# Optimization experiments

Hardware: AMD Instinct MI355X
Metric: run time of the kernel (lower is better)

## Reference

```python
import jax, jax.numpy as jnp
import numpy as np

N = 16384        # total atoms
E = 262144       # edges
D = 128          # dim_embedding
F = 128          # num_filters
G = 50           # num_gaussians
L = 4            # num_interactions
CUTOFF = 5.0
GAMMA = 4.0
NUM_MOLS = 32
LOG2 = float(np.log(2.0))


def ssp(x):
    # ShiftedSoftplus: softplus(x) - log(2)
    return jax.nn.softplus(x) - LOG2


def setup_inputs() -> dict:
    key = jax.random.key(0)
    ks = jax.random.split(key, 24)
    s = lambda *sh: 1.0 / np.sqrt(sh[-2]) if len(sh) >= 2 else 0.1
    inp = {
        "z": jax.random.normal(ks[0], (N, 1), jnp.float32),
        "pos": jax.random.uniform(ks[1], (N, 3), jnp.float32),
        "batch": jnp.sort(jax.random.randint(ks[2], (N,), 0, NUM_MOLS)),
        "edge_src": jax.random.randint(ks[3], (E,), 0, N),
        "edge_dst": jax.random.randint(ks[4], (E,), 0, N),
        # embedding Linear(1, D)
        "emb_W": jax.random.normal(ks[5], (1, D), jnp.float32),
        "emb_b": jax.random.normal(ks[6], (D,), jnp.float32) * 0.1,
        # per-interaction stacked params [L, ...]
        "mlp_W1": jax.random.normal(ks[7], (L, G, F), jnp.float32) / np.sqrt(G),
        "mlp_b1": jnp.zeros((L, F), jnp.float32),
        "mlp_W2": jax.random.normal(ks[8], (L, F, F), jnp.float32) / np.sqrt(F),
        "mlp_b2": jnp.zeros((L, F), jnp.float32),
        "cf1_W": jax.random.normal(ks[9], (L, D, F), jnp.float32) / np.sqrt(D),   # CFConv.lin1 (no bias)
        "cf2_W": jax.random.normal(ks[10], (L, F, D), jnp.float32) / np.sqrt(F),  # CFConv.lin2
        "cf2_b": jnp.zeros((L, D), jnp.float32),
        "int_lin_W": jax.random.normal(ks[11], (L, D, D), jnp.float32) / np.sqrt(D),
        "int_lin_b": jnp.zeros((L, D), jnp.float32),
        # readout head
        "lin1_W": jax.random.normal(ks[12], (D, D // 2), jnp.float32) / np.sqrt(D),
        "lin1_b": jnp.zeros((D // 2,), jnp.float32),
        "lin2_W": jax.random.normal(ks[13], (D // 2, 1), jnp.float32) / np.sqrt(D // 2),
        "lin2_b": jnp.zeros((1,), jnp.float32),
    }
    return inp


def reference(z, pos, batch, edge_src, edge_dst, emb_W, emb_b,
              mlp_W1, mlp_b1, mlp_W2, mlp_b2, cf1_W, cf2_W, cf2_b,
              int_lin_W, int_lin_b, lin1_W, lin1_b, lin2_W, lin2_b):
    # atom embedding: Linear(1, D)
    h = z @ emb_W + emb_b                                  # [N, D]

    # interaction graph distances (graph connectivity precomputed)
    diff = pos[edge_src] - pos[edge_dst]                   # [E, 3]
    dist = jnp.sqrt(jnp.sum(diff * diff, axis=-1) + 1e-12) # [E]

    # radial basis expansion
    mu = jnp.linspace(0.0, CUTOFF, G).astype(h.dtype)      # [G]
    rbf = jnp.exp(-GAMMA * (dist[:, None] - mu) ** 2)      # [E, G]

    # cosine cutoff envelope
    C = 0.5 * (jnp.cos(dist * (np.pi / CUTOFF)) + 1.0)     # [E]

    for l in range(L):
        # continuous filter from RBF: MLP [E,G] -> [E,F]
        Wf = ssp(rbf @ mlp_W1[l] + mlp_b1[l]) @ mlp_W2[l] + mlp_b2[l]
        Wf = Wf * C[:, None]                               # [E, F]
        # CFConv: gather - multiply - scatter-add
        xj = (h @ cf1_W[l])[edge_src]                      # [E, F]
        agg = jax.ops.segment_sum(xj * Wf, edge_dst, num_segments=N)  # [N, F]
        x = agg @ cf2_W[l] + cf2_b[l]                      # [N, D]
        x = ssp(x)
        x = x @ int_lin_W[l] + int_lin_b[l]
        h = h + x                                          # residual

    h = ssp(h @ lin1_W + lin1_b) @ lin2_W + lin2_b         # [N, 1]
    out = jax.ops.segment_sum(h, batch, num_segments=NUM_MOLS)  # [NUM_MOLS, 1]
    return out
```

## Files before the change

kernel.cpp:

```cpp
#include <hip/hip_runtime.h>
#include <hip/hip_bf16.h>
#include <math.h>

#define N_ATOMS 16384
#define N_EDGES 262144
#define DIM 128
#define NF 128
#define NG 50
#define NL 4
#define NMOLS 32
#define EW 8

typedef short bf16x8 __attribute__((ext_vector_type(8)));
typedef float f32x4 __attribute__((ext_vector_type(4)));

__device__ __forceinline__ float ssp_f(float x) {
    float e = __expf(-fabsf(x));
    return fmaxf(x, 0.0f) + __logf(1.0f + e) - 0.6931471805599453f;
}

__device__ __forceinline__ short f2bf(float x) {
    __hip_bfloat16 b = __float2bfloat16(x);
    return *reinterpret_cast<short*>(&b);
}

__device__ __forceinline__ float bf2f(unsigned short u) {
    unsigned int v = ((unsigned int)u) << 16;
    return __builtin_bit_cast(float, v);
}

__global__ __launch_bounds__(512)
void k_embed_geom(const float* __restrict__ z, const float* __restrict__ Wv,
                  const float* __restrict__ bv, float* __restrict__ h,
                  const float* __restrict__ pos, const int* __restrict__ src,
                  const int* __restrict__ dst, float* __restrict__ dist,
                  float* __restrict__ Cenv, int* __restrict__ deg) {
    int idx = blockIdx.x * 512 + threadIdx.x;
    int n = idx >> 7, d = idx & 127;
    h[idx] = z[n] * Wv[d] + bv[d];
    if (blockIdx.x < N_EDGES / 512) {
        int e = blockIdx.x * 512 + threadIdx.x;
        int s = src[e], t = dst[e];
        float dx = pos[3*s]   - pos[3*t];
        float dy = pos[3*s+1] - pos[3*t+1];
        float dz = pos[3*s+2] - pos[3*t+2];
        float dd = sqrtf(dx*dx + dy*dy + dz*dz + 1e-12f);
        dist[e] = dd;
        Cenv[e] = 0.5f * (cosf(dd * (float)(M_PI / 5.0)) + 1.0f);
        atomicAdd(&deg[t], 1);
    }
}

__global__ __launch_bounds__(1024)
void k_scan(const int* __restrict__ deg, int* __restrict__ cur) {
    __shared__ int tot[1024];
    int t = threadIdx.x;
    int v[16];
    int s = 0;
    #pragma unroll
    for (int j = 0; j < 16; ++j) { int x = deg[t * 16 + j]; v[j] = s; s += x; }
    tot[t] = s;
    __syncthreads();
    for (int off = 1; off < 1024; off <<= 1) {
        int add = (t >= off) ? tot[t - off] : 0;
        __syncthreads();
        tot[t] += add;
        __syncthreads();
    }
    int base = (t == 0) ? 0 : tot[t - 1];
    #pragma unroll
    for (int j = 0; j < 16; ++j) cur[t * 16 + j] = base + v[j];
}

__global__ void k_fill(const int* __restrict__ dst, int* __restrict__ cur,
                       int* __restrict__ edge_of) {
    int e = blockIdx.x * blockDim.x + threadIdx.x;
    if (e < N_EDGES) {
        int p = atomicAdd(&cur[dst[e]], 1);
        edge_of[p] = e;
    }
}

__global__ __launch_bounds__(512)
void k_perm_rbf(const int* __restrict__ edge_of, const float* __restrict__ dist,
                const float* __restrict__ Cenv, const int* __restrict__ src,
                const int* __restrict__ dst, float* __restrict__ CenvS,
                int* __restrict__ srcS, int* __restrict__ dstS,
                short* __restrict__ rbfF) {
    int p = blockIdx.x * blockDim.x + threadIdx.x;
    if (p >= N_EDGES) return;
    int e = edge_of[p];
    float d = dist[e];
    CenvS[p] = Cenv[e];
    srcS[p]  = src[e];
    dstS[p]  = dst[e];
    int t = p >> 4, m = p & 15;
    #pragma unroll
    for (int kc = 0; kc < 2; ++kc) {
        #pragma unroll
        for (int q = 0; q < 4; ++q) {
            bf16x8 v;
            #pragma unroll
            for (int j = 0; j < 8; ++j) {
                float mu = (float)(kc * 32 + q * 8 + j) * (5.0f / 49.0f);
                float tt = d - mu;
                v[j] = f2bf(__expf(-4.0f * tt * tt));
            }
            *(bf16x8*)&rbfF[(size_t)((t * 2 + kc) * 64 + q * 16 + m) * 8] = v;
        }
    }
}

__global__ __launch_bounds__(512, 4)
void k_edge_csr(const short* __restrict__ rbfF, const float* __restrict__ CenvS,
                const int* __restrict__ srcS, const int* __restrict__ dstS,
                const float* __restrict__ W1, const float* __restrict__ b1,
                const float* __restrict__ W2, const float* __restrict__ b2,
                const unsigned short* __restrict__ xjb, float* __restrict__ agg)
{
    __shared__ short H1s[64 * 128];
    __shared__ unsigned short msgt[64][136];
    __shared__ int dsts[64];
    __shared__ unsigned long long maskS;
    const int tid  = threadIdx.x;
    const int lane = tid & 63;
    const int w    = tid >> 6;
    const int q    = lane >> 4;
    const int m    = lane & 15;

    bf16x8 W1R[2], W2R[4];
    #pragma unroll
    for (int kc = 0; kc < 2; ++kc) {
        bf16x8 f;
        #pragma unroll
        for (int j = 0; j < 8; ++j) {
            int k = kc * 32 + q * 8 + j;
            float v = (k < NG) ? W1[k * NF + w * 16 + m] : 0.0f;
            f[j] = f2bf(v);
        }
        W1R[kc] = f;
    }
    #pragma unroll
    for (int kc = 0; kc < 4; ++kc) {
        bf16x8 f;
        #pragma unroll
        for (int j = 0; j < 8; ++j) {
            int k = kc * 32 + q * 8 + j;
            f[j] = f2bf(W2[k * NF + w * 16 + m]);
        }
        W2R[kc] = f;
    }
    const float b1v = b1[w * 16 + m];
    const float b2v = b2[w * 16 + m];

    const int nrounds = N_EDGES / 64;
    for (int r = blockIdx.x; r < nrounds; r += gridDim.x) {
        const int p0 = r * 64;
        short* H = H1s;

        #pragma unroll
        for (int a = 0; a < 4; ++a) {
            int tile = r * 4 + a;
            f32x4 acc = {b1v, b1v, b1v, b1v};
            #pragma unroll
            for (int kc = 0; kc < 2; ++kc) {
                bf16x8 A = *(const bf16x8*)&rbfF[(size_t)((tile * 2 + kc) * 64 + lane) * 8];
                acc = __builtin_amdgcn_mfma_f32_16x16x32_bf16(A, W1R[kc], acc, 0, 0, 0);
            }
            #pragma unroll
            for (int i = 0; i < 4; ++i) {
                int e = a * 16 + q * 4 + i;
                int f = w * 16 + m;
                int byte = (e * 256 + f * 2) ^ ((e & 7) << 4);
                *(short*)((char*)H + byte) = f2bf(ssp_f(acc[i]));
            }
        }
        __syncthreads();

        unsigned short xu[4][4];
        #pragma unroll
        for (int a = 0; a < 4; ++a) {
            int4 s4 = *(const int4*)&srcS[p0 + a * 16 + q * 4];
            #pragma unroll
            for (int i = 0; i < 4; ++i)
                xu[a][i] = xjb[(size_t)((const int*)&s4)[i] * NF + w * 16 + m];
        }

        f32x4 acc2[4];
        #pragma unroll
        for (int a = 0; a < 4; ++a) {
            f32x4 acc = {b2v, b2v, b2v, b2v};
            #pragma unroll
            for (int kc = 0; kc < 4; ++kc) {
                int e = a * 16 + m;
                int byte = (e * 256 + (kc * 32 + q * 8) * 2) ^ ((e & 7) << 4);
                bf16x8 A = *(const bf16x8*)((const char*)H + byte);
                acc = __builtin_amdgcn_mfma_f32_16x16x32_bf16(A, W2R[kc], acc, 0, 0, 0);
            }
            acc2[a] = acc;
        }

        #pragma unroll
        for (int a = 0; a < 4; ++a) {
            float4 cc4 = *(const float4*)&CenvS[p0 + a * 16 + q * 4];
            #pragma unroll
            for (int i = 0; i < 4; ++i) {
                float v = acc2[a][i] * ((const float*)&cc4)[i];
                msgt[a * 16 + q * 4 + i][w * 16 + m] =
                    (unsigned short)f2bf(v * bf2f(xu[a][i]));
            }
        }
        if (w == 0) {
            int d = dstS[p0 + lane];
            int prev = __shfl_up(d, 1);
            bool head = (lane == 0) || (d != prev);
            unsigned long long mk = __ballot(head);
            dsts[lane] = d;
            if (lane == 0) maskS = mk;
        }
        __syncthreads();

        {
            int f = tid & 127;
            int g = tid >> 7;
            unsigned long long mm = maskS;
            int k = 0;
            while (mm) {
                int start = __ffsll(mm) - 1;
                mm &= mm - 1;
                int end = mm ? (__ffsll(mm) - 1) : 64;
                if ((k & 3) == g) {
                    float s0 = 0.0f, s1 = 0.0f, s2 = 0.0f, s3 = 0.0f;
                    int p = start;
                    for (; p + 4 <= end; p += 4) {
                        s0 += bf2f(msgt[p    ][f]);
                        s1 += bf2f(msgt[p + 1][f]);
                        s2 += bf2f(msgt[p + 2][f]);
                        s3 += bf2f(msgt[p + 3][f]);
                    }
                    for (; p < end; ++p) s0 += bf2f(msgt[p][f]);
                    float s = (s0 + s1) + (s2 + s3);
                    float* addr = &agg[(size_t)dsts[start] * NF + f];
                    if (start == 0 || end == 64) atomicAdd(addr, s);
                    else *addr = s;
                }
                ++k;
            }
        }
    }
}

template<int ACT, int RESID, int OUTBF>
__global__ __launch_bounds__(512, 2)
void k_node_mfma(const float* __restrict__ in, const float* __restrict__ W,
                 const float* __restrict__ bias, const float* __restrict__ resid,
                 void* __restrict__ outv, float* __restrict__ aggz)
{
    __shared__ short T[32 * 128];
    const int tid  = threadIdx.x;
    const int lane = tid & 63;
    const int w    = tid >> 6;
    const int q    = lane >> 4;
    const int m    = lane & 15;

    bf16x8 WR[4];
    #pragma unroll
    for (int kc = 0; kc < 4; ++kc) {
        bf16x8 f;
        #pragma unroll
        for (int j = 0; j < 8; ++j)
            f[j] = f2bf(W[(kc * 32 + q * 8 + j) * DIM + w * 16 + m]);
        WR[kc] = f;
    }
    const float bv = bias ? bias[w * 16 + m] : 0.0f;

    const int r0 = blockIdx.x * 32;

    {
        int row = tid >> 4;
        int k0  = (tid & 15) * 8;
        const float* src = in + (size_t)(r0 + row) * DIM + k0;
        float4 v0 = *(const float4*)(src);
        float4 v1 = *(const float4*)(src + 4);
        bf16x8 lo;
        #pragma unroll
        for (int j = 0; j < 4; ++j) {
            lo[j]     = f2bf(((const float*)&v0)[j]);
            lo[j + 4] = f2bf(((const float*)&v1)[j]);
        }
        int b0 = (row * 256 + k0 * 2) ^ ((row & 7) << 4);
        *(bf16x8*)((char*)T + b0) = lo;
        if (aggz) {
            float4 zz = {0.0f, 0.0f, 0.0f, 0.0f};
            float* dz = aggz + (size_t)(r0 + row) * DIM + k0;
            *(float4*)dz = zz;
            *(float4*)(dz + 4) = zz;
        }
    }
    __syncthreads();

    #pragma unroll
    for (int a = 0; a < 2; ++a) {
        f32x4 acc = {bv, bv, bv, bv};
        int row = a * 16 + m;
        #pragma unroll
        for (int kc = 0; kc < 4; ++kc) {
            int byte = (row * 256 + (kc * 32 + q * 8) * 2) ^ ((row & 7) << 4);
            bf16x8 A = *(const bf16x8*)((const char*)T + byte);
            acc = __builtin_amdgcn_mfma_f32_16x16x32_bf16(A, WR[kc], acc, 0, 0, 0);
        }
        #pragma unroll
        for (int i = 0; i < 4; ++i) {
            float v = acc[i];
            if (ACT) v = ssp_f(v);
            size_t oi = (size_t)(r0 + a * 16 + q * 4 + i) * DIM + w * 16 + m;
            if (RESID) v += resid[oi];
            if (OUTBF) ((unsigned short*)outv)[oi] = (unsigned short)f2bf(v);
            else       ((float*)outv)[oi] = v;
        }
    }
}

template<int EMIT, int FINAL>
__global__ __launch_bounds__(512, 2)
void k_node_fused(const float* __restrict__ agg, const float* __restrict__ W2,
                  const float* __restrict__ b2, const float* __restrict__ Wi,
                  const float* __restrict__ bi, float* __restrict__ h,
                  const float* __restrict__ W1n, unsigned short* __restrict__ xjn,
                  float* __restrict__ aggz,
                  const float* __restrict__ l1W, const float* __restrict__ l1B,
                  const float* __restrict__ l2W, const float* __restrict__ l2b,
                  const int* __restrict__ batch, float* __restrict__ out)
{
    __shared__ short T[32 * 128];
    __shared__ short X[32 * 128];
    __shared__ float part[32][4];
    __shared__ float molsS[NMOLS];
    const int tid  = threadIdx.x;
    const int lane = tid & 63;
    const int w    = tid >> 6;
    const int q    = lane >> 4;
    const int m    = lane & 15;

    if (FINAL && tid < NMOLS) molsS[tid] = 0.0f;

    bf16x8 W2R[4], WiR[4], W1nR[4], L1R[4];
    #pragma unroll
    for (int kc = 0; kc < 4; ++kc) {
        bf16x8 f2v, fiv;
        #pragma unroll
        for (int j = 0; j < 8; ++j) {
            int k = kc * 32 + q * 8 + j;
            f2v[j] = f2bf(W2[k * DIM + w * 16 + m]);
            fiv[j] = f2bf(Wi[k * DIM + w * 16 + m]);
        }
        W2R[kc] = f2v;
        WiR[kc] = fiv;
    }
    if constexpr (EMIT) {
        #pragma unroll
        for (int kc = 0; kc < 4; ++kc) {
            bf16x8 f;
            #pragma unroll
            for (int j = 0; j < 8; ++j)
                f[j] = f2bf(W1n[(kc * 32 + q * 8 + j) * DIM + w * 16 + m]);
            W1nR[kc] = f;
        }
    }
    if constexpr (FINAL) {
        if (w < 4) {
            #pragma unroll
            for (int kc = 0; kc < 4; ++kc) {
                bf16x8 f;
                #pragma unroll
                for (int j = 0; j < 8; ++j)
                    f[j] = f2bf(l1W[(kc * 32 + q * 8 + j) * 64 + w * 16 + m]);
                L1R[kc] = f;
            }
        }
    }
    const float b2v = b2[w * 16 + m];
    const float biv = bi[w * 16 + m];

    const int r0 = blockIdx.x * 32;
    const int srow = tid >> 4;
    const int sk0  = (tid & 15) * 8;

    {
        const float* src = agg + (size_t)(r0 + srow) * DIM + sk0;
        float4 v0 = *(const float4*)(src);
        float4 v1 = *(const float4*)(src + 4);
        bf16x8 lo;
        #pragma unroll
        for (int j = 0; j < 4; ++j) {
            lo[j]     = f2bf(((const float*)&v0)[j]);
            lo[j + 4] = f2bf(((const float*)&v1)[j]);
        }
        int b0 = (srow * 256 + sk0 * 2) ^ ((srow & 7) << 4);
        *(bf16x8*)((char*)T + b0) = lo;
    }
    __syncthreads();

    #pragma unroll
    for (int a = 0; a < 2; ++a) {
        f32x4 acc = {b2v, b2v, b2v, b2v};
        int row = a * 16 + m;
        #pragma unroll
        for (int kc = 0; kc < 4; ++kc) {
            int byte = (row * 256 + (kc * 32 + q * 8) * 2) ^ ((row & 7) << 4);
            bf16x8 A = *(const bf16x8*)((const char*)T + byte);
            acc = __builtin_amdgcn_mfma_f32_16x16x32_bf16(A, W2R[kc], acc, 0, 0, 0);
        }
        #pragma unroll
        for (int i = 0; i < 4; ++i) {
            int orow = a * 16 + q * 4 + i;
            int ocol = w * 16 + m;
            int byte = (orow * 256 + ocol * 2) ^ ((orow & 7) << 4);
            *(short*)((char*)X + byte) = f2bf(ssp_f(acc[i]));
        }
    }
    __syncthreads();

    #pragma unroll
    for (int a = 0; a < 2; ++a) {
        f32x4 acc = {biv, biv, biv, biv};
        int row = a * 16 + m;
        #pragma unroll
        for (int kc = 0; kc < 4; ++kc) {
            int byte = (row * 256 + (kc * 32 + q * 8) * 2) ^ ((row & 7) << 4);
            bf16x8 A = *(const bf16x8*)((const char*)X + byte);
            acc = __builtin_amdgcn_mfma_f32_16x16x32_bf16(A, WiR[kc], acc, 0, 0, 0);
        }
        #pragma unroll
        for (int i = 0; i < 4; ++i) {
            size_t oi = (size_t)(r0 + a * 16 + q * 4 + i) * DIM + w * 16 + m;
            float v = h[oi] + acc[i];
            h[oi] = v;
            if constexpr (EMIT || FINAL) {
                int orow = a * 16 + q * 4 + i;
                int ocol = w * 16 + m;
                int byte = (orow * 256 + ocol * 2) ^ ((orow & 7) << 4);
                *(short*)((char*)T + byte) = f2bf(v);
            }
        }
    }

    if constexpr (EMIT) {
        float4 zz = {0.0f, 0.0f, 0.0f, 0.0f};
        float* dz = aggz + (size_t)(r0 + srow) * DIM + sk0;
        *(float4*)dz = zz;
        *(float4*)(dz + 4) = zz;
    }
    if constexpr (EMIT || FINAL) __syncthreads();

    if constexpr (EMIT) {
        #pragma unroll
        for (int a = 0; a < 2; ++a) {
            f32x4 acc = {0.0f, 0.0f, 0.0f, 0.0f};
            int row = a * 16 + m;
            #pragma unroll
            for (int kc = 0; kc < 4; ++kc) {
                int byte = (row * 256 + (kc * 32 + q * 8) * 2) ^ ((row & 7) << 4);
                bf16x8 A = *(const bf16x8*)((const char*)T + byte);
                acc = __builtin_amdgcn_mfma_f32_16x16x32_bf16(A, W1nR[kc], acc, 0, 0, 0);
            }
            #pragma unroll
            for (int i = 0; i < 4; ++i) {
                size_t oi = (size_t)(r0 + a * 16 + q * 4 + i) * DIM + w * 16 + m;
                xjn[oi] = (unsigned short)f2bf(acc[i]);
            }
        }
    }

    if constexpr (FINAL) {
        if (w < 4) {
            const float l1bv = l1B[w * 16 + m];
            const float l2wv = l2W[w * 16 + m];
            #pragma unroll
            for (int a = 0; a < 2; ++a) {
                f32x4 acc = {l1bv, l1bv, l1bv, l1bv};
                int row = a * 16 + m;
                #pragma unroll
                for (int kc = 0; kc < 4; ++kc) {
                    int byte = (row * 256 + (kc * 32 + q * 8) * 2) ^ ((row & 7) << 4);
                    bf16x8 A = *(const bf16x8*)((const char*)T + byte);
                    acc = __builtin_amdgcn_mfma_f32_16x16x32_bf16(A, L1R[kc], acc, 0, 0, 0);
                }
                #pragma unroll
                for (int i = 0; i < 4; ++i) {
                    float v = ssp_f(acc[i]) * l2wv;
                    #pragma unroll
                    for (int off = 1; off < 16; off <<= 1) v += __shfl_xor(v, off);
                    if (m == 0) part[a * 16 + q * 4 + i][w] = v;
                }
            }
        }
        __syncthreads();
        if (tid < 32) {
            float s = part[tid][0] + part[tid][1] + part[tid][2] + part[tid][3] + l2b[0];
            atomicAdd(&molsS[batch[r0 + tid]], s);
        }
        __syncthreads();
        if (tid < NMOLS) {
            float v = molsS[tid];
            if (v != 0.0f) atomicAdd(&out[tid], v);
        }
    }
}

extern "C" void kernel_launch(void* const* d_in, const int* in_sizes, int n_in,
                              void* d_out, int out_size, void* d_ws, size_t ws_size,
                              hipStream_t stream) {
    const float* z     = (const float*)d_in[0];
    const float* pos   = (const float*)d_in[1];
    const int*   batch = (const int*)d_in[2];
    const int*   esrc  = (const int*)d_in[3];
    const int*   edst  = (const int*)d_in[4];
    const float* embW  = (const float*)d_in[5];
    const float* embB  = (const float*)d_in[6];
    const float* mlpW1 = (const float*)d_in[7];
    const float* mlpB1 = (const float*)d_in[8];
    const float* mlpW2 = (const float*)d_in[9];
    const float* mlpB2 = (const float*)d_in[10];
    const float* cf1W  = (const float*)d_in[11];
    const float* cf2W  = (const float*)d_in[12];
    const float* cf2B  = (const float*)d_in[13];
    const float* intW  = (const float*)d_in[14];
    const float* intB  = (const float*)d_in[15];
    const float* l1W   = (const float*)d_in[16];
    const float* l1B   = (const float*)d_in[17];
    const float* l2W   = (const float*)d_in[18];
    const float* l2B   = (const float*)d_in[19];
    float* out = (float*)d_out;

    char* ws = (char*)d_ws;
    float* h     = (float*)(ws);
    float* dist  = (float*)(ws + (size_t)( 8 << 20));
    float* Cv    = (float*)(ws + (size_t)( 9 << 20));
    unsigned short* xj = (unsigned short*)(ws + (size_t)(10 << 20));
    float* agg   = (float*)(ws + (size_t)(18 << 20));
    short* rbfF  = (short*)(ws + (size_t)(26 << 20));
    int*   deg   = (int*)  (ws + (size_t)(58 << 20));
    int*   cur   = (int*)  (ws + (size_t)(59 << 20));
    int*   edge_of = (int*)(ws + (size_t)(60 << 20));
    float* CenvS = (float*)(ws + (size_t)(62 << 20));
    int*   srcS  = (int*)  (ws + (size_t)(63 << 20));
    int*   dstS  = (int*)  (ws + (size_t)(64 << 20));

    hipMemsetAsync(deg, 0, N_ATOMS * sizeof(int), stream);
    hipMemsetAsync(out, 0, NMOLS * sizeof(float), stream);

    k_embed_geom<<<dim3(N_ATOMS * DIM / 512), dim3(512), 0, stream>>>(
        z, embW, embB, h, pos, esrc, edst, dist, Cv, deg);
    k_scan<<<dim3(1), dim3(1024), 0, stream>>>(deg, cur);
    k_fill<<<dim3(N_EDGES / 512), dim3(512), 0, stream>>>(edst, cur, edge_of);
    k_perm_rbf<<<dim3(N_EDGES / 512), dim3(512), 0, stream>>>(
        edge_of, dist, Cv, esrc, edst, CenvS, srcS, dstS, rbfF);

    k_node_mfma<0, 0, 1><<<dim3(N_ATOMS / 32), dim3(512), 0, stream>>>(
        h, cf1W, nullptr, nullptr, (void*)xj, agg);

    for (int l = 0; l < NL; ++l) {
        k_edge_csr<<<dim3(1024), dim3(512), 0, stream>>>(
            rbfF, CenvS, srcS, dstS,
            mlpW1 + (size_t)l * NG * NF, mlpB1 + (size_t)l * NF,
            mlpW2 + (size_t)l * NF * NF, mlpB2 + (size_t)l * NF,
            xj, agg);
        if (l < NL - 1) {
            k_node_fused<1, 0><<<dim3(N_ATOMS / 32), dim3(512), 0, stream>>>(
                agg, cf2W + (size_t)l * NF * DIM, cf2B + (size_t)l * DIM,
                intW + (size_t)l * DIM * DIM, intB + (size_t)l * DIM, h,
                cf1W + (size_t)(l + 1) * DIM * NF, xj, agg,
                nullptr, nullptr, nullptr, nullptr, nullptr, nullptr);
        } else {
            k_node_fused<0, 1><<<dim3(N_ATOMS / 32), dim3(512), 0, stream>>>(
                agg, cf2W + (size_t)l * NF * DIM, cf2B + (size_t)l * DIM,
                intW + (size_t)l * DIM * DIM, intB + (size_t)l * DIM, h,
                nullptr, nullptr, nullptr,
                l1W, l1B, l2W, l2B, batch, out);
        }
    }
}
```

Baseline: 449.2 us.

## Double-buffer edge LDS tile and make segment reduction wave-local to drop a barrier

The hidden-activation LDS buffer is now double-buffered, so the next round's first MLP stage can overwrite it without waiting for slow waves. Each wave computes the destination-run mask itself with a ballot and reduces only its own 16 filter columns across the four lane quads using shuffles. This removes the shared dsts/mask arrays and one __syncthreads per round. The edge grid also shrinks from 1024 to 768 blocks, which may suit the extra LDS use. In exchange, every wave walks all runs and does shuffle reductions, and each thread loads dstS redundantly.

```diff
diff --git a/kernel.cpp b/kernel.cpp
--- a/kernel.cpp
+++ b/kernel.cpp
@@ -118,10 +118,8 @@
                 const float* __restrict__ W2, const float* __restrict__ b2,
                 const unsigned short* __restrict__ xjb, float* __restrict__ agg)
 {
-    __shared__ short H1s[64 * 128];
+    __shared__ short H1s[2][64 * 128];
     __shared__ unsigned short msgt[64][136];
-    __shared__ int dsts[64];
-    __shared__ unsigned long long maskS;
     const int tid  = threadIdx.x;
     const int lane = tid & 63;
     const int w    = tid >> 6;
@@ -154,9 +152,10 @@
     const float b2v = b2[w * 16 + m];
 
     const int nrounds = N_EDGES / 64;
-    for (int r = blockIdx.x; r < nrounds; r += gridDim.x) {
+    int rb = 0;
+    for (int r = blockIdx.x; r < nrounds; r += gridDim.x, ++rb) {
         const int p0 = r * 64;
-        short* H = H1s;
+        short* H = H1s[rb & 1];
 
         #pragma unroll
         for (int a = 0; a < 4; ++a) {
@@ -175,7 +174,11 @@
                 *(short*)((char*)H + byte) = f2bf(ssp_f(acc[i]));
             }
         }
-        __syncthreads();
+
+        int dstv = dstS[p0 + lane];
+        int prev = __shfl_up(dstv, 1);
+        bool head = (lane == 0) || (dstv != prev);
+        unsigned long long mk = __ballot(head);
 
         unsigned short xu[4][4];
         #pragma unroll
@@ -185,6 +188,8 @@
             for (int i = 0; i < 4; ++i)
                 xu[a][i] = xjb[(size_t)((const int*)&s4)[i] * NF + w * 16 + m];
         }
+
+        __syncthreads();
 
         f32x4 acc2[4];
         #pragma unroll
@@ -210,41 +215,26 @@
                     (unsigned short)f2bf(v * bf2f(xu[a][i]));
             }
         }
-        if (w == 0) {
-            int d = dstS[p0 + lane];
-            int prev = __shfl_up(d, 1);
-            bool head = (lane == 0) || (d != prev);
-            unsigned long long mk = __ballot(head);
-            dsts[lane] = d;
-            if (lane == 0) maskS = mk;
-        }
-        __syncthreads();
 
         {
-            int f = tid & 127;
-            int g = tid >> 7;
-            unsigned long long mm = maskS;
-            int k = 0;
+            unsigned long long mm = mk;
             while (mm) {
                 int start = __ffsll(mm) - 1;
                 mm &= mm - 1;
                 int end = mm ? (__ffsll(mm) - 1) : 64;
-                if ((k & 3) == g) {
-                    float s0 = 0.0f, s1 = 0.0f, s2 = 0.0f, s3 = 0.0f;
-                    int p = start;
-                    for (; p + 4 <= end; p += 4) {
-                        s0 += bf2f(msgt[p    ][f]);
-                        s1 += bf2f(msgt[p + 1][f]);
-                        s2 += bf2f(msgt[p + 2][f]);
-                        s3 += bf2f(msgt[p + 3][f]);
-                    }
-                    for (; p < end; ++p) s0 += bf2f(msgt[p][f]);
-                    float s = (s0 + s1) + (s2 + s3);
-                    float* addr = &agg[(size_t)dsts[start] * NF + f];
+                int drun = __shfl(dstv, start);
+                int lo = max(start, q * 16);
+                int hi = min(end, q * 16 + 16);
+                float s = 0.0f;
+                for (int p = lo; p < hi; ++p)
+                    s += bf2f(msgt[p][w * 16 + m]);
+                s += __shfl_xor(s, 16);
+                s += __shfl_xor(s, 32);
+                if (q == 0) {
+                    float* addr = &agg[(size_t)drun * NF + w * 16 + m];
                     if (start == 0 || end == 64) atomicAdd(addr, s);
                     else *addr = s;
                 }
-                ++k;
             }
         }
     }
@@ -561,7 +551,7 @@
         h, cf1W, nullptr, nullptr, (void*)xj, agg);
 
     for (int l = 0; l < NL; ++l) {
-        k_edge_csr<<<dim3(1024), dim3(512), 0, stream>>>(
+        k_edge_csr<<<dim3(768), dim3(512), 0, stream>>>(
             rbfF, CenvS, srcS, dstS,
             mlpW1 + (size_t)l * NG * NF, mlpB1 + (size_t)l * NF,
             mlpW2 + (size_t)l * NF * NF, mlpB2 + (size_t)l * NF,
```

Measured after the change: 594.9 us. +32.4%, slower.
